# Kernel optimization log

Measured on AMD Instinct MI355X. Metric: run time of the kernel, lower is better.

## Reference

```python
import jax, jax.numpy as jnp
import numpy as np


def setup_inputs() -> dict:
    key = jax.random.key(0)
    k1, k2, k3, k4, k5, k6 = jax.random.split(key, 6)
    B, L, D, V = 4096, 128, 64, 1000
    return {
        "src_ids": jax.random.randint(k1, (B, L), 0, V),
        "dst_ids": jax.random.randint(k2, (B, L), 0, V),
        "W1": jax.random.normal(k3, (1, D), jnp.float32),
        "b1": jax.random.normal(k4, (D,), jnp.float32),
        "W2": jax.random.normal(k5, (D, D), jnp.float32),
        "b2": jax.random.normal(k6, (D, D)[:1] + (D,), jnp.float32)[0] if False else jax.random.normal(k6, (D,), jnp.float32),
    }


def _pair_counts(a, b):
    # counts[bt, i] = number of j with b[bt, j] == a[bt, i]  -> (B, La)
    return (a[:, :, None] == b[:, None, :]).sum(axis=-1).astype(jnp.float32)


def _encode_and_pool(appear, W1, b1, W2, b2):
    # appear: (B, L, 2) counts. MLP on each scalar count, then sum over the 2 channels.
    h = jax.nn.relu(appear[..., None] * W1[0] + b1)      # (B, L, 2, D)
    feat = (jnp.einsum("blcd,de->blce", h, W2) + b2).sum(axis=2)  # (B, L, D)
    L = feat.shape[1]
    w = jnp.exp(jnp.arange(L, dtype=jnp.float32) - L)    # exp(x - k), k = L
    # exponential-weighted mean over the sequence dim
    return (feat * w[None, :, None]).sum(axis=1) / w.sum()  # (B, D)


def reference(src_ids, dst_ids, W1, b1, W2, b2):
    # per-row co-occurrence counts (hash-join expressed as masked pairwise equality)
    src_in_src = _pair_counts(src_ids, src_ids)
    src_in_dst = _pair_counts(src_ids, dst_ids)
    dst_in_src = _pair_counts(dst_ids, src_ids)
    dst_in_dst = _pair_counts(dst_ids, dst_ids)
    src_app = jnp.stack([src_in_src, src_in_dst], axis=-1)  # (B, Ls, 2)
    dst_app = jnp.stack([dst_in_src, dst_in_dst], axis=-1)  # (B, Ld, 2)
    # zero out padding positions (neighbor id == 0)
    src_app = jnp.where((src_ids == 0)[..., None], 0.0, src_app)
    dst_app = jnp.where((dst_ids == 0)[..., None], 0.0, dst_app)
    src_feat = _encode_and_pool(src_app, W1, b1, W2, b2)
    dst_feat = _encode_and_pool(dst_app, W1, b1, W2, b2)
    return src_feat, dst_feat
```

## Files before the change

### kernel.cpp

```cpp
#include <hip/hip_runtime.h>

#define LSEQ 128
#define DIM  64
#define NCNT 129
#define TAIL 16

__global__ __launch_bounds__(256) void build_table_kernel(
        const float* __restrict__ W1,
        const float* __restrict__ b1,
        const float* __restrict__ W2,
        float* __restrict__ G) {
    const int c = blockIdx.x * 4 + (threadIdx.x >> 6);
    const int d = threadIdx.x & (DIM - 1);
    if (c >= NCNT) return;
    const float fc = (float)c;
    float acc = 0.0f;
#pragma unroll
    for (int k = 0; k < DIM; ++k) {
        float h = fmaxf(fmaf(fc, W1[k], b1[k]), 0.0f);
        acc = fmaf(h, W2[k * DIM + d], acc);
    }
    G[c * DIM + d] = acc;
}

__global__ __launch_bounds__(256) void gae_kernel(
        const int* __restrict__ src_ids,
        const int* __restrict__ dst_ids,
        const float* __restrict__ G,
        const float* __restrict__ b2,
        float* __restrict__ out,
        int B) {
    const int lane = threadIdx.x & 63;
    const int g    = threadIdx.x >> 6;
    const int sel  = g & 1;
    const int row  = blockIdx.x * 2 + (g >> 1);
    if (row >= B) return;

    const int* __restrict__ sp = src_ids + (size_t)row * LSEQ;
    const int* __restrict__ dp = dst_ids + (size_t)row * LSEQ;
    const int s_lo = sp[lane];
    const int s_hi = sp[lane + 64];
    const int d_lo = dp[lane];
    const int d_hi = dp[lane + 64];
    const int my_hi = sel ? d_hi : s_hi;

    float w   = expf((float)-TAIL);
    float acc = 0.0f;
#pragma unroll
    for (int i = 0; i < TAIL; ++i) {
        const int l = LSEQ - TAIL + i;
        const int v = __shfl(my_hi, l - 64, 64);
        int c0 = __popcll(__ballot(s_lo == v)) + __popcll(__ballot(s_hi == v));
        int c1 = __popcll(__ballot(d_lo == v)) + __popcll(__ballot(d_hi == v));
        if (v == 0) { c0 = 0; c1 = 0; }
        const float g0 = G[c0 * DIM + lane];
        const float g1 = G[c1 * DIM + lane];
        acc = fmaf(w, g0 + g1, acc);
        w *= 2.71828182845904523f;
    }

    const float invW = 1.71828182845904523f;
    out[(size_t)sel * B * DIM + (size_t)row * DIM + lane] =
        acc * invW + 2.0f * b2[lane];
}

extern "C" void kernel_launch(void* const* d_in, const int* in_sizes, int n_in,
                              void* d_out, int out_size, void* d_ws, size_t ws_size,
                              hipStream_t stream) {
    const int*   src_ids = (const int*)d_in[0];
    const int*   dst_ids = (const int*)d_in[1];
    const float* W1      = (const float*)d_in[2];
    const float* b1      = (const float*)d_in[3];
    const float* W2      = (const float*)d_in[4];
    const float* b2      = (const float*)d_in[5];
    float*       out     = (float*)d_out;
    float*       G       = (float*)d_ws;

    const int B = in_sizes[0] / LSEQ;

    build_table_kernel<<<(NCNT + 3) / 4, 256, 0, stream>>>(W1, b1, W2, G);
    gae_kernel<<<(B + 1) / 2, 256, 0, stream>>>(src_ids, dst_ids, G, b2, out, B);
}
```

Baseline: 70.90 us.

## Fuse table build into main kernel by reassociating W2 after weighted pooling

Removes the separate lookup-table kernel and instead accumulates the exponentially weighted ReLU hidden activations per lane, then applies W2 once per row via readlane broadcasts. This drops one kernel launch and the per-step table gathers, in exchange for a 64x64 matrix-vector product per row reading W2 from cache. The shuffle of the query id is also replaced with readlane since the source lane is uniform.

```diff
diff --git a/kernel.cpp b/kernel.cpp
--- a/kernel.cpp
+++ b/kernel.cpp
@@ -2,31 +2,14 @@
 
 #define LSEQ 128
 #define DIM  64
-#define NCNT 129
 #define TAIL 16
 
-__global__ __launch_bounds__(256) void build_table_kernel(
+__global__ __launch_bounds__(256) void gae_fused_kernel(
+        const int* __restrict__ src_ids,
+        const int* __restrict__ dst_ids,
         const float* __restrict__ W1,
         const float* __restrict__ b1,
         const float* __restrict__ W2,
-        float* __restrict__ G) {
-    const int c = blockIdx.x * 4 + (threadIdx.x >> 6);
-    const int d = threadIdx.x & (DIM - 1);
-    if (c >= NCNT) return;
-    const float fc = (float)c;
-    float acc = 0.0f;
-#pragma unroll
-    for (int k = 0; k < DIM; ++k) {
-        float h = fmaxf(fmaf(fc, W1[k], b1[k]), 0.0f);
-        acc = fmaf(h, W2[k * DIM + d], acc);
-    }
-    G[c * DIM + d] = acc;
-}
-
-__global__ __launch_bounds__(256) void gae_kernel(
-        const int* __restrict__ src_ids,
-        const int* __restrict__ dst_ids,
-        const float* __restrict__ G,
         const float* __restrict__ b2,
         float* __restrict__ out,
         int B) {
@@ -36,6 +19,9 @@
     const int row  = blockIdx.x * 2 + (g >> 1);
     if (row >= B) return;
 
+    const float w1k = W1[lane];
+    const float b1k = b1[lane];
+
     const int* __restrict__ sp = src_ids + (size_t)row * LSEQ;
     const int* __restrict__ dp = dst_ids + (size_t)row * LSEQ;
     const int s_lo = sp[lane];
@@ -44,24 +30,33 @@
     const int d_hi = dp[lane + 64];
     const int my_hi = sel ? d_hi : s_hi;
 
-    float w   = expf((float)-TAIL);
-    float acc = 0.0f;
+    float w = 1.12535174719259115e-7f;
+    float S = 0.0f;
 #pragma unroll
     for (int i = 0; i < TAIL; ++i) {
         const int l = LSEQ - TAIL + i;
-        const int v = __shfl(my_hi, l - 64, 64);
+        const int v = __builtin_amdgcn_readlane(my_hi, l - 64);
         int c0 = __popcll(__ballot(s_lo == v)) + __popcll(__ballot(s_hi == v));
         int c1 = __popcll(__ballot(d_lo == v)) + __popcll(__ballot(d_hi == v));
         if (v == 0) { c0 = 0; c1 = 0; }
-        const float g0 = G[c0 * DIM + lane];
-        const float g1 = G[c1 * DIM + lane];
-        acc = fmaf(w, g0 + g1, acc);
+        const float r0 = fmaxf(fmaf((float)c0, w1k, b1k), 0.0f);
+        const float r1 = fmaxf(fmaf((float)c1, w1k, b1k), 0.0f);
+        S = fmaf(w, r0 + r1, S);
         w *= 2.71828182845904523f;
+    }
+
+    float acc0 = 0.0f, acc1 = 0.0f;
+#pragma unroll
+    for (int k = 0; k < DIM; k += 2) {
+        const float sk0 = __uint_as_float(__builtin_amdgcn_readlane(__float_as_uint(S), k));
+        const float sk1 = __uint_as_float(__builtin_amdgcn_readlane(__float_as_uint(S), k + 1));
+        acc0 = fmaf(sk0, W2[k * DIM + lane], acc0);
+        acc1 = fmaf(sk1, W2[(k + 1) * DIM + lane], acc1);
     }
 
     const float invW = 1.71828182845904523f;
     out[(size_t)sel * B * DIM + (size_t)row * DIM + lane] =
-        acc * invW + 2.0f * b2[lane];
+        (acc0 + acc1) * invW + 2.0f * b2[lane];
 }
 
 extern "C" void kernel_launch(void* const* d_in, const int* in_sizes, int n_in,
@@ -74,10 +69,10 @@
     const float* W2      = (const float*)d_in[4];
     const float* b2      = (const float*)d_in[5];
     float*       out     = (float*)d_out;
-    float*       G       = (float*)d_ws;
+    (void)d_ws; (void)ws_size;
 
     const int B = in_sizes[0] / LSEQ;
 
-    build_table_kernel<<<(NCNT + 3) / 4, 256, 0, stream>>>(W1, b1, W2, G);
-    gae_kernel<<<(B + 1) / 2, 256, 0, stream>>>(src_ids, dst_ids, G, b2, out, B);
+    gae_fused_kernel<<<(B + 1) / 2, 256, 0, stream>>>(
+        src_ids, dst_ids, W1, b1, W2, b2, out, B);
 }
```

New measurement: 69.16 us. 1.03x faster.
